# Performance work log

Hardware: AMD Instinct MI355X
Metric: run time of the kernel (lower is better)

## Reference

```python
import jax, jax.numpy as jnp
import numpy as np

EPS = 1e-05
# log-space init values matching the torch module (deterministic: use the means)
_S_MEANS = np.array([0.61803, 0.3904, 0.1174, 0.0606, 0.0308, 0.0155, 0.0078, 0.0039, 0.002, 0.0001], dtype=np.float32)


def setup_inputs() -> dict:
    key = jax.random.key(0)
    k1, k2 = jax.random.split(key)
    B, F, T = 16, 128, 2048
    x = jax.random.uniform(k1, (B, F, T), dtype=jnp.float32)  # nonneg spectrogram-like
    # perturb s means slightly like torch.normal(mean, 0.01*mean)
    noise = 1.0 + 0.01 * jax.random.normal(k2, (10,), dtype=jnp.float32)
    s_log = jnp.log(jnp.abs(jnp.asarray(_S_MEANS) * noise))
    alpha_log = jnp.full((F,), jnp.log(0.8), dtype=jnp.float32)
    delta_log = jnp.full((F,), jnp.log(10.0), dtype=jnp.float32)
    r_log = jnp.full((F,), jnp.log(0.25), dtype=jnp.float32)
    return {"x": x, "s_log": s_log, "alpha_log": alpha_log, "delta_log": delta_log, "r_log": r_log}


def _pcen(x, s_log, alpha_log, delta_log, r_log):
    # x: [B, F, T]
    s = jnp.exp(s_log)[:, None, None]        # [10,1,1]
    alpha = jnp.exp(alpha_log)[:, None]      # [F,1]
    delta = jnp.exp(delta_log)[:, None]      # [F,1]
    r = jnp.exp(r_log)[:, None]              # [F,1]

    x_t = jnp.moveaxis(x, -1, 0)             # [T, B, F]
    init = jnp.broadcast_to(x_t[0][None], (10,) + x_t[0].shape)  # [10,B,F]

    def step(carry, xt):
        carry = (1.0 - s) * carry + s * xt[None]  # [10,B,F]
        return carry, carry

    _, rest = jax.lax.scan(step, init, x_t[1:])
    smoother = jnp.concatenate([init[None], rest], axis=0)   # [T,10,B,F]
    smoother = jnp.moveaxis(smoother, 0, -1)                 # [10,B,F,T]

    log_eps = jnp.log(jnp.float32(EPS))
    smooth = jnp.exp(-alpha * (log_eps + jnp.log1p(smoother / EPS)))  # [10,B,F,T]
    pcen = (x[None] * smooth + delta) ** r - delta ** r              # [10,B,F,T]
    return jnp.transpose(pcen, (1, 0, 2, 3))                          # [B,10,F,T]


def reference(x, s_log, alpha_log, delta_log, r_log):
    return _pcen(x, s_log, alpha_log, delta_log, r_log)
```

## Files before the change

### kernel.cpp

```cpp
#include <hip/hip_runtime.h>

#define T_DIM 2048
#define F_DIM 128
#define B_DIM 16
#define NS 10
#define NTILE 8
#define TPB 256

__device__ __forceinline__ float fast_exp2(float x) { return __builtin_amdgcn_exp2f(x); }
__device__ __forceinline__ float fast_log2(float x) { return __builtin_amdgcn_logf(x); }

__global__ __launch_bounds__(TPB) void pcen_kernel(
    const float* __restrict__ x,
    const float* __restrict__ s_log,
    const float* __restrict__ alpha_log,
    const float* __restrict__ delta_log,
    const float* __restrict__ r_log,
    float* __restrict__ out)
{
    const int tid  = threadIdx.x;
    const int lane = tid & 63;
    const int gw   = blockIdx.x * (TPB / 64) + (tid >> 6);
    const int bf   = gw / NS;
    const int si   = gw - bf * NS;
    const int b    = bf >> 7;
    const int f    = bf & (F_DIM - 1);

    const float4* xrow = (const float4*)(x + (size_t)bf * T_DIM);

    float4 xv[NTILE];
    #pragma unroll
    for (int k = 0; k < NTILE; ++k) xv[k] = xrow[k * 64 + lane];

    const float s  = expf(s_log[si]);
    const float a  = 1.0f - s;
    const float alpha = expf(alpha_log[f]);
    const float delta = expf(delta_log[f]);
    const float r     = expf(r_log[f]);
    const float delta_r   = fast_exp2(r * fast_log2(delta));
    const float neg_alpha = -alpha;

    float pa[6];
    {
        float a2 = a * a;
        pa[0] = a2 * a2;
        #pragma unroll
        for (int bb = 1; bb < 6; ++bb) pa[bb] = pa[bb - 1] * pa[bb - 1];
    }
    const float a256 = pa[5] * pa[5];

    float a4l = 1.0f;
    #pragma unroll
    for (int bb = 0; bb < 6; ++bb) a4l *= ((lane >> bb) & 1) ? pa[bb] : 1.0f;

    float V[NTILE];
    #pragma unroll
    for (int k = 0; k < NTILE; ++k) {
        float c = s * xv[k].x;
        c = fmaf(a, c, s * xv[k].y);
        c = fmaf(a, c, s * xv[k].z);
        c = fmaf(a, c, s * xv[k].w);
        V[k] = c;
    }

    #pragma unroll
    for (int d = 1, bb = 0; d < 64; d <<= 1, ++bb) {
        #pragma unroll
        for (int k = 0; k < NTILE; ++k) {
            float up = __shfl_up(V[k], d);
            up = (lane >= d) ? up : 0.0f;
            V[k] = fmaf(pa[bb], up, V[k]);
        }
    }

    float Ve[NTILE], Vl[NTILE];
    #pragma unroll
    for (int k = 0; k < NTILE; ++k) {
        float e = __shfl_up(V[k], 1);
        Ve[k] = (lane >= 1) ? e : 0.0f;
        Vl[k] = __shfl(V[k], 63);
    }

    float tc = __shfl(xv[0].x, 0);

    float* orow = out + (size_t)(((b * NS + si) * F_DIM) + f) * T_DIM;

    #pragma unroll
    for (int k = 0; k < NTILE; ++k) {
        float cc = fmaf(a4l, tc, Ve[k]);
        const float4 xk = xv[k];
        float4 o;

        cc = fmaf(a, cc, s * xk.x);
        { float sm2 = fast_exp2(neg_alpha * fast_log2(cc + 1e-5f));
          float base = fmaf(xk.x, sm2, delta);
          o.x = fast_exp2(r * fast_log2(base)) - delta_r; }

        cc = fmaf(a, cc, s * xk.y);
        { float sm2 = fast_exp2(neg_alpha * fast_log2(cc + 1e-5f));
          float base = fmaf(xk.y, sm2, delta);
          o.y = fast_exp2(r * fast_log2(base)) - delta_r; }

        cc = fmaf(a, cc, s * xk.z);
        { float sm2 = fast_exp2(neg_alpha * fast_log2(cc + 1e-5f));
          float base = fmaf(xk.z, sm2, delta);
          o.z = fast_exp2(r * fast_log2(base)) - delta_r; }

        cc = fmaf(a, cc, s * xk.w);
        { float sm2 = fast_exp2(neg_alpha * fast_log2(cc + 1e-5f));
          float base = fmaf(xk.w, sm2, delta);
          o.w = fast_exp2(r * fast_log2(base)) - delta_r; }

        tc = fmaf(a256, tc, Vl[k]);

        ((float4*)orow)[k * 64 + lane] = o;
    }
}

extern "C" void kernel_launch(void* const* d_in, const int* in_sizes, int n_in,
                              void* d_out, int out_size, void* d_ws, size_t ws_size,
                              hipStream_t stream) {
    const float* x         = (const float*)d_in[0];
    const float* s_log     = (const float*)d_in[1];
    const float* alpha_log = (const float*)d_in[2];
    const float* delta_log = (const float*)d_in[3];
    const float* r_log     = (const float*)d_in[4];
    float* out = (float*)d_out;

    const int total_waves = B_DIM * F_DIM * NS;
    const int blocks = total_waves / (TPB / 64);

    pcen_kernel<<<dim3(blocks), dim3(TPB), 0, stream>>>(
        x, s_log, alpha_log, delta_log, r_log, out);
}
```

Measured before the change: 188.8 us.

## Cut register pressure by reloading x, add occupancy hint and nontemporal stores

The kernel no longer keeps all eight float4 x tiles in registers. It reloads each tile from global memory (expected to hit cache) in the output phase and computes the shuffles for each tile on the fly. It also requests 8 waves per SIMD via launch_bounds, replaces expf with a native exp2-based exp for the parameters, and writes the large output with nontemporal stores so it bypasses cache pollution. The intent is higher occupancy and less cache traffic from the write-dominated output, at the cost of a second read of x.

```diff
diff --git a/kernel.cpp b/kernel.cpp
--- a/kernel.cpp
+++ b/kernel.cpp
@@ -7,10 +7,13 @@
 #define NTILE 8
 #define TPB 256
 
+typedef float floatx4 __attribute__((ext_vector_type(4)));
+
 __device__ __forceinline__ float fast_exp2(float x) { return __builtin_amdgcn_exp2f(x); }
 __device__ __forceinline__ float fast_log2(float x) { return __builtin_amdgcn_logf(x); }
+__device__ __forceinline__ float fast_exp(float x) { return fast_exp2(x * 1.44269504088896340736f); }
 
-__global__ __launch_bounds__(TPB) void pcen_kernel(
+__global__ __launch_bounds__(TPB, 8) void pcen_kernel(
     const float* __restrict__ x,
     const float* __restrict__ s_log,
     const float* __restrict__ alpha_log,
@@ -28,15 +31,11 @@
 
     const float4* xrow = (const float4*)(x + (size_t)bf * T_DIM);
 
-    float4 xv[NTILE];
-    #pragma unroll
-    for (int k = 0; k < NTILE; ++k) xv[k] = xrow[k * 64 + lane];
-
-    const float s  = expf(s_log[si]);
+    const float s  = fast_exp(s_log[si]);
     const float a  = 1.0f - s;
-    const float alpha = expf(alpha_log[f]);
-    const float delta = expf(delta_log[f]);
-    const float r     = expf(r_log[f]);
+    const float alpha = fast_exp(alpha_log[f]);
+    const float delta = fast_exp(delta_log[f]);
+    const float r     = fast_exp(r_log[f]);
     const float delta_r   = fast_exp2(r * fast_log2(delta));
     const float neg_alpha = -alpha;
 
@@ -54,12 +53,15 @@
     for (int bb = 0; bb < 6; ++bb) a4l *= ((lane >> bb) & 1) ? pa[bb] : 1.0f;
 
     float V[NTILE];
+    float x0;
     #pragma unroll
     for (int k = 0; k < NTILE; ++k) {
-        float c = s * xv[k].x;
-        c = fmaf(a, c, s * xv[k].y);
-        c = fmaf(a, c, s * xv[k].z);
-        c = fmaf(a, c, s * xv[k].w);
+        float4 xk = xrow[k * 64 + lane];
+        if (k == 0) x0 = __shfl(xk.x, 0);
+        float c = s * xk.x;
+        c = fmaf(a, c, s * xk.y);
+        c = fmaf(a, c, s * xk.z);
+        c = fmaf(a, c, s * xk.w);
         V[k] = c;
     }
 
@@ -73,23 +75,20 @@
         }
     }
 
-    float Ve[NTILE], Vl[NTILE];
-    #pragma unroll
-    for (int k = 0; k < NTILE; ++k) {
-        float e = __shfl_up(V[k], 1);
-        Ve[k] = (lane >= 1) ? e : 0.0f;
-        Vl[k] = __shfl(V[k], 63);
-    }
-
-    float tc = __shfl(xv[0].x, 0);
+    float tc = x0;
 
     float* orow = out + (size_t)(((b * NS + si) * F_DIM) + f) * T_DIM;
+    floatx4* orow4 = (floatx4*)orow;
 
     #pragma unroll
     for (int k = 0; k < NTILE; ++k) {
-        float cc = fmaf(a4l, tc, Ve[k]);
-        const float4 xk = xv[k];
-        float4 o;
+        float Ve = __shfl_up(V[k], 1);
+        Ve = (lane >= 1) ? Ve : 0.0f;
+        const float Vl = __shfl(V[k], 63);
+
+        float cc = fmaf(a4l, tc, Ve);
+        const float4 xk = xrow[k * 64 + lane];
+        floatx4 o;
 
         cc = fmaf(a, cc, s * xk.x);
         { float sm2 = fast_exp2(neg_alpha * fast_log2(cc + 1e-5f));
@@ -111,9 +110,9 @@
           float base = fmaf(xk.w, sm2, delta);
           o.w = fast_exp2(r * fast_log2(base)) - delta_r; }
 
-        tc = fmaf(a256, tc, Vl[k]);
+        tc = fmaf(a256, tc, Vl);
 
-        ((float4*)orow)[k * 64 + lane] = o;
+        __builtin_nontemporal_store(o, &orow4[k * 64 + lane]);
     }
 }
 
```

Result: slower. 213.2 us (+12.9%).
